# Optimization experiments

Measured on AMD Instinct MI355X. Metric: run time of the kernel, lower is better.

## Reference

```python
import jax, jax.numpy as jnp
import numpy as np

B, S, D_IN, D_H = 8, 4096, 256, 512
EPS = 1e-6


def setup_inputs() -> dict:
    key = jax.random.key(0)
    ks = jax.random.split(key, 5)
    scale = 1.0 / np.sqrt(D_IN)  # torch Linear default init scale (uniform bound)
    x = jax.random.normal(ks[0], (B, S, D_IN), dtype=jnp.float32)
    Wi = jax.random.normal(ks[1], (D_IN, D_H), dtype=jnp.float32) * scale
    Wf = jax.random.normal(ks[2], (D_IN, D_H), dtype=jnp.float32) * scale
    Wo = jax.random.normal(ks[3], (D_IN, D_H), dtype=jnp.float32) * scale
    Wz = jax.random.normal(ks[4], (D_IN, D_H), dtype=jnp.float32) * scale
    zb = jnp.zeros((D_H,), dtype=jnp.float32)
    return {"x": x, "Wi": Wi, "bi": zb, "Wf": Wf, "bf": zb,
            "Wo": Wo, "bo": zb, "Wz": Wz, "bz": zb}


def _xlstm_forward(x, Wi, bi, Wf, bf, Wo, bo, Wz, bz):
    # Batched projections over all timesteps at once: [B,S,D_H] each.
    i_t = jnp.exp(jnp.clip(jnp.einsum('bsd,dh->bsh', x, Wi) + bi, -20.0, 0.0))
    f_t = jnp.exp(jnp.clip(jnp.einsum('bsd,dh->bsh', x, Wf) + bf, -20.0, 0.0))
    o_t = jax.nn.sigmoid(jnp.einsum('bsd,dh->bsh', x, Wo) + bo)
    z_t = jnp.tanh(jnp.einsum('bsd,dh->bsh', x, Wz) + bz)

    def step(carry, gates):
        c, n = carry
        i, f, o, z = gates
        c = f * c + i * z
        n = f * n + i
        h = o * (c / (n + EPS))
        return (c, n), h

    c0 = jnp.zeros((x.shape[0], Wi.shape[1]), dtype=x.dtype)
    n0 = jnp.ones((x.shape[0], Wi.shape[1]), dtype=x.dtype)
    # time-major scan over the recurrence
    gates_tm = tuple(jnp.swapaxes(g, 0, 1) for g in (i_t, f_t, o_t, z_t))  # [S,B,H]
    _, h_tm = jax.lax.scan(step, (c0, n0), gates_tm)
    return jnp.swapaxes(h_tm, 0, 1)  # [B,S,H]


def reference(x, Wi, bi, Wf, bf, Wo, bo, Wz, bz):
    return _xlstm_forward(x, Wi, bi, Wf, bf, Wo, bo, Wz, bz)
```

## Files before the change

kernel.cpp:

```cpp
#include <hip/hip_runtime.h>
#include <hip/hip_bf16.h>
#include <cstdint>
#include <cstddef>

typedef __hip_bfloat16 bf16;
typedef __attribute__((ext_vector_type(8))) short short8;
typedef __attribute__((ext_vector_type(4))) short short4v;
typedef __attribute__((ext_vector_type(4))) float floatx4;

#define BB 8
#define SS 4096
#define DIN 256
#define DH 512
#define NCH 256
#define CHUNK 16

__device__ __forceinline__ float b2f(bf16 v) { return __bfloat162float(v); }
__device__ __forceinline__ float sh2f(short v) {
    unsigned int u = ((unsigned int)(unsigned short)v) << 16;
    float f; __builtin_memcpy(&f, &u, 4); return f;
}
__device__ __forceinline__ float frcp(float x) { return __builtin_amdgcn_rcpf(x); }
__device__ __forceinline__ short f2sh(float a) {
    bf16 bv = __float2bfloat16(a);
    short sv; __builtin_memcpy(&sv, &bv, 2); return sv;
}

__global__ __launch_bounds__(256) void convert_x(
    const float* __restrict__ X, bf16* __restrict__ Xb)
{
    const int idx = blockIdx.x * 256 + threadIdx.x;
    float4 v = ((const float4*)X)[idx];
    bf16 o[4] = {__float2bfloat16(v.x), __float2bfloat16(v.y),
                 __float2bfloat16(v.z), __float2bfloat16(v.w)};
    ((short4v*)Xb)[idx] = *(const short4v*)o;
}

__global__ __launch_bounds__(256) void transpose_w(
    const float* __restrict__ Wi, const float* __restrict__ Wf,
    const float* __restrict__ Wo, const float* __restrict__ Wz,
    bf16* __restrict__ Wt)
{
    int o = blockIdx.x * 256 + threadIdx.x;
    int r = o >> 8;
    int k = o & 255;
    int y = r >> 7;
    int c = r & 127;
    int g = c >> 5;
    int h = y * 32 + (c & 31);
    const float* W = (g == 0) ? Wi : (g == 1) ? Wf : (g == 2) ? Wo : Wz;
    Wt[o] = __float2bfloat16(W[(size_t)k * DH + h]);
}

__device__ __forceinline__ void load16_lds(const bf16* g, short* l)
{
    __builtin_amdgcn_global_load_lds(
        (const __attribute__((address_space(1))) unsigned int*)g,
        (__attribute__((address_space(3))) unsigned int*)l,
        16, 0, 0);
}

__global__ __launch_bounds__(256) void gemm_mfma(
    const bf16* __restrict__ Xb, const bf16* __restrict__ Wt,
    const float* __restrict__ bi, const float* __restrict__ bfv,
    const float* __restrict__ bo, const float* __restrict__ bz,
    bf16* __restrict__ Pi, bf16* __restrict__ Pf,
    bf16* __restrict__ Po, bf16* __restrict__ Pz,
    float* __restrict__ Aa, float* __restrict__ Bca, float* __restrict__ Bna,
    int nb)
{
    __shared__ __align__(16) short smem[128 * 132];

    const int tid  = threadIdx.x;
    const int y    = blockIdx.x;
    const int m0   = blockIdx.y * 128;
    const int n0   = y * 128;
    const int wave = tid >> 6, lane = tid & 63;
    const int wm   = (wave >> 1) * 64, wn = (wave & 1) * 64;
    const int l15  = lane & 15;
    const int q    = lane >> 4;

    floatx4 acc[4][4];
#pragma unroll
    for (int i = 0; i < 4; i++)
#pragma unroll
        for (int j = 0; j < 4; j++) acc[i][j] = (floatx4){0.f, 0.f, 0.f, 0.f};

    const int r_ld = tid >> 2;
    const int c_ld = tid & 3;
    const bf16* agp0 = Xb + (size_t)(m0 + r_ld) * DIN + c_ld * 8;
    const bf16* agp1 = Xb + (size_t)(m0 + 64 + r_ld) * DIN + c_ld * 8;
    const bf16* bgp0 = Wt + (size_t)(n0 + r_ld) * DIN + c_ld * 8;
    const bf16* bgp1 = Wt + (size_t)(n0 + 64 + r_ld) * DIN + c_ld * 8;

#define STAGE(K0, BUF)                                            \
    do {                                                          \
        short* A_ = smem + (BUF) * 8192;                          \
        short* B_ = A_ + 4096;                                    \
        load16_lds(agp0 + (K0), &A_[tid * 8]);                    \
        load16_lds(agp1 + (K0), &A_[2048 + tid * 8]);             \
        load16_lds(bgp0 + (K0), &B_[tid * 8]);                    \
        load16_lds(bgp1 + (K0), &B_[2048 + tid * 8]);             \
    } while (0)

    STAGE(0, 0);
    asm volatile("s_waitcnt vmcnt(0)" ::: "memory");
    __builtin_amdgcn_s_barrier();

#pragma unroll
    for (int k = 0; k < 8; k++) {
        const int cur = k & 1;
        if (k < 7) STAGE((k + 1) * 32, cur ^ 1);
        const short* A = smem + cur * 8192;
        const short* B = A + 4096;
        short8 af[4], bfr[4];
#pragma unroll
        for (int ti = 0; ti < 4; ti++)
            af[ti] = *(const short8*)&A[(wm + ti * 16 + l15) * 32 + q * 8];
#pragma unroll
        for (int tj = 0; tj < 4; tj++)
            bfr[tj] = *(const short8*)&B[(wn + tj * 16 + l15) * 32 + q * 8];
#pragma unroll
        for (int ti = 0; ti < 4; ti++)
#pragma unroll
            for (int tj = 0; tj < 4; tj++)
                acc[ti][tj] = __builtin_amdgcn_mfma_f32_16x16x32_bf16(
                    af[ti], bfr[tj], acc[ti][tj], 0, 0, 0);
        asm volatile("s_waitcnt vmcnt(0) lgkmcnt(0)" ::: "memory");
        __builtin_amdgcn_s_barrier();
    }
#undef STAGE

#pragma unroll
    for (int ti = 0; ti < 4; ti++) {
        const int mrow = wm + ti * 16 + q * 4;
#pragma unroll
        for (int tj = 0; tj < 4; tj++) {
            const int cb = wn + tj * 16;
            const int g  = cb >> 5;
            const int c  = cb + l15;
            const float* bp = (g == 0) ? bi : (g == 1) ? bfv
                            : (g == 2) ? bo : bz;
            const float bsv = bp[y * 32 + (c & 31)];
#pragma unroll
            for (int r = 0; r < 4; r++) {
                const float v = acc[ti][tj][r] + bsv;
                float a;
                if (g == 0 || g == 1) {
                    a = __expf(fminf(fmaxf(v, -20.f), 0.f));
                } else if (g == 2) {
                    a = frcp(1.f + __expf(-v));
                } else {
                    a = 1.f - 2.f * frcp(__expf(2.f * v) + 1.f);
                }
                smem[(mrow + r) * 132 + c] = f2sh(a);
            }
        }
    }
    __syncthreads();

    const int bidx = m0 / SS;

    {
        const int cp  = (tid & 31) * 4;
        const int g2  = cp >> 5;
        const int hb  = y * 32 + (cp & 31);
        bf16* pl = ((g2 == 0) ? Pi : (g2 == 1) ? Pf : (g2 == 2) ? Po : Pz) + hb;
        const int r0 = tid >> 5;
#pragma unroll
        for (int t = 0; t < 16; t++) {
            const int row = t * 8 + r0;
            short4v v = *(const short4v*)&smem[row * 132 + cp];
            *(short4v*)(pl + (size_t)(m0 + row) * DH) = v;
        }
    }

    {
        const int hh = tid & 31;
        const int ch = tid >> 5;
        float A = 1.f, Bc = 0.f, Bn = 0.f;
        const short* base = &smem[(ch * CHUNK) * 132];
#pragma unroll
        for (int s = 0; s < CHUNK; s++) {
            const short* rp = base + s * 132;
            const float iv = sh2f(rp[hh]);
            const float f  = sh2f(rp[32 + hh]);
            const float zv = sh2f(rp[96 + hh]);
            Bc = fmaf(f, Bc, iv * zv);
            Bn = fmaf(f, Bn, iv);
            A *= f;
        }
        const int ch_g = ((m0 % SS) >> 4) + ch;
        const int hgl  = y * 32 + hh;
        const size_t cidx = (size_t)(ch_g * nb + bidx) * DH + hgl;
        Aa[cidx] = A; Bca[cidx] = Bc; Bna[cidx] = Bn;
    }
}

__global__ __launch_bounds__(256) void scan_chunks(
    float* __restrict__ Aa, float* __restrict__ Bca,
    const float* __restrict__ Bna, int nb)
{
    const int t = blockIdx.x * 256 + threadIdx.x;
    float c = 0.f, n = 1.f;
    for (int ch = 0; ch < NCH; ch++) {
        const size_t cidx = (size_t)ch * (nb * DH) + t;
        const float A  = Aa[cidx];
        const float Bc = Bca[cidx];
        const float Bn = Bna[cidx];
        Aa[cidx] = c; Bca[cidx] = n;
        c = fmaf(A, c, Bc);
        n = fmaf(A, n, Bn);
    }
}

__global__ __launch_bounds__(256) void scan_emit(
    const bf16* __restrict__ Pi, const bf16* __restrict__ Pf,
    const bf16* __restrict__ Po, const bf16* __restrict__ Pz,
    const float* __restrict__ Cs, const float* __restrict__ Ns,
    float* __restrict__ out, int nb)
{
    const int tid = threadIdx.x;
    const int ch  = blockIdx.x * 4 + (tid >> 6);
    const int b   = blockIdx.y;
    const int hg  = (tid & 63) * 8;
    const size_t base = ((size_t)(b * SS + ch * CHUNK)) * DH + hg;
    const size_t cidx = (size_t)(ch * nb + b) * DH + hg;

    float c[8], n[8];
#pragma unroll
    for (int j = 0; j < 2; j++) {
        *(floatx4*)&c[j * 4] = *(const floatx4*)(Cs + cidx + j * 4);
        *(floatx4*)&n[j * 4] = *(const floatx4*)(Ns + cidx + j * 4);
    }

#pragma unroll 4
    for (int s = 0; s < CHUNK; s++) {
        const size_t o = base + (size_t)s * DH;
        short8 i8 = *(const short8*)(Pi + o);
        short8 f8 = *(const short8*)(Pf + o);
        short8 o8 = *(const short8*)(Po + o);
        short8 z8 = *(const short8*)(Pz + o);
        float h[8];
#pragma unroll
        for (int j = 0; j < 8; j++) {
            const float f  = sh2f(f8[j]);
            const float iv = sh2f(i8[j]);
            const float ov = sh2f(o8[j]);
            const float zv = sh2f(z8[j]);
            c[j] = fmaf(f, c[j], iv * zv);
            n[j] = fmaf(f, n[j], iv);
            h[j] = ov * c[j] * frcp(n[j] + 1e-6f);
        }
        *(floatx4*)(out + o)     = *(floatx4*)&h[0];
        *(floatx4*)(out + o + 4) = *(floatx4*)&h[4];
    }
}

extern "C" void kernel_launch(void* const* d_in, const int* in_sizes, int n_in,
                              void* d_out, int out_size, void* d_ws, size_t ws_size,
                              hipStream_t stream)
{
    const float* x   = (const float*)d_in[0];
    const float* Wi  = (const float*)d_in[1];
    const float* bi  = (const float*)d_in[2];
    const float* Wf  = (const float*)d_in[3];
    const float* bfv = (const float*)d_in[4];
    const float* Wo  = (const float*)d_in[5];
    const float* bo  = (const float*)d_in[6];
    const float* Wz  = (const float*)d_in[7];
    const float* bz  = (const float*)d_in[8];
    float* out = (float*)d_out;

    int nb = BB;
    while (nb > 1) {
        size_t need = (1u << 20)
                    + (size_t)nb * SS * DIN * 2
                    + 4 * (size_t)nb * SS * DH * 2
                    + 3 * (size_t)NCH * nb * DH * 4;
        if (need <= ws_size) break;
        nb >>= 1;
    }

    const size_t plane = (size_t)nb * SS * DH;
    bf16* Wt = (bf16*)d_ws;
    bf16* Xb = (bf16*)((char*)d_ws + (1u << 20));
    bf16* Pi = Xb + (size_t)nb * SS * DIN;
    bf16* Pf = Pi + plane;
    bf16* Po = Pf + plane;
    bf16* Pz = Po + plane;
    float* Aa  = (float*)(Pz + plane);
    float* Bca = Aa  + (size_t)NCH * nb * DH;
    float* Bna = Bca + (size_t)NCH * nb * DH;

    transpose_w<<<2048, 256, 0, stream>>>(Wi, Wf, Wo, Wz, Wt);

    for (int b0 = 0; b0 < BB; b0 += nb) {
        const float* Xsrc = x   + (size_t)b0 * SS * DIN;
        float*       Ob   = out + (size_t)b0 * SS * DH;
        convert_x<<<nb * 1024, 256, 0, stream>>>(Xsrc, Xb);
        gemm_mfma<<<dim3(16, nb * SS / 128), 256, 0, stream>>>(
            Xb, Wt, bi, bfv, bo, bz, Pi, Pf, Po, Pz, Aa, Bca, Bna, nb);
        scan_chunks<<<2 * nb, 256, 0, stream>>>(Aa, Bca, Bna, nb);
        scan_emit<<<dim3(NCH / 4, nb), 256, 0, stream>>>(
            Pi, Pf, Po, Pz, Aa, Bca, Ob, nb);
    }
}
```

Measured before the change: 253.9 us.

## Triple-buffer GEMM loads, swizzle block order, parallelize chunk scan, widen emit grid

The GEMM moves from double to triple buffering with partial vmcnt waits, so global-to-LDS loads for two stages ahead overlap the MFMA work. It also remaps block indices across 8 groups, likely an XCD-aware swizzle. The chunk-state scan splits its 256 chunks into 4 segments per hidden lane and combines them through shared memory, giving more blocks and a shorter serial chain. scan_emit now handles 4 channels per thread with twice as many blocks, trading narrower vector loads for more parallelism.

```diff
diff --git a/kernel.cpp b/kernel.cpp
--- a/kernel.cpp
+++ b/kernel.cpp
@@ -69,12 +69,15 @@
     float* __restrict__ Aa, float* __restrict__ Bca, float* __restrict__ Bna,
     int nb)
 {
-    __shared__ __align__(16) short smem[128 * 132];
+    __shared__ __align__(16) short smem[3 * 8192];
+
+    const int cpx = gridDim.x >> 3;
+    const int logical = ((int)blockIdx.x & 7) * cpx + ((int)blockIdx.x >> 3);
+    const int y  = logical & 15;
+    const int m0 = (logical >> 4) * 128;
+    const int n0 = y * 128;
 
     const int tid  = threadIdx.x;
-    const int y    = blockIdx.x;
-    const int m0   = blockIdx.y * 128;
-    const int n0   = y * 128;
     const int wave = tid >> 6, lane = tid & 63;
     const int wm   = (wave >> 1) * 64, wn = (wave & 1) * 64;
     const int l15  = lane & 15;
@@ -104,14 +107,18 @@
     } while (0)
 
     STAGE(0, 0);
-    asm volatile("s_waitcnt vmcnt(0)" ::: "memory");
-    __builtin_amdgcn_s_barrier();
+    STAGE(32, 1);
 
 #pragma unroll
     for (int k = 0; k < 8; k++) {
-        const int cur = k & 1;
-        if (k < 7) STAGE((k + 1) * 32, cur ^ 1);
-        const short* A = smem + cur * 8192;
+        if (k < 6) STAGE((k + 2) * 32, (k + 2) % 3);
+        if (k < 6)       asm volatile("s_waitcnt vmcnt(8)" ::: "memory");
+        else if (k == 6) asm volatile("s_waitcnt vmcnt(4)" ::: "memory");
+        else             asm volatile("s_waitcnt vmcnt(0)" ::: "memory");
+        __builtin_amdgcn_s_barrier();
+        __builtin_amdgcn_sched_barrier(0);
+
+        const short* A = smem + (k % 3) * 8192;
         const short* B = A + 4096;
         short8 af[4], bfr[4];
 #pragma unroll
@@ -126,7 +133,8 @@
             for (int tj = 0; tj < 4; tj++)
                 acc[ti][tj] = __builtin_amdgcn_mfma_f32_16x16x32_bf16(
                     af[ti], bfr[tj], acc[ti][tj], 0, 0, 0);
-        asm volatile("s_waitcnt vmcnt(0) lgkmcnt(0)" ::: "memory");
+        asm volatile("s_waitcnt lgkmcnt(0)" ::: "memory");
+        __builtin_amdgcn_sched_barrier(0);
         __builtin_amdgcn_s_barrier();
     }
 #undef STAGE
@@ -201,16 +209,46 @@
     float* __restrict__ Aa, float* __restrict__ Bca,
     const float* __restrict__ Bna, int nb)
 {
-    const int t = blockIdx.x * 256 + threadIdx.x;
+    __shared__ float sA[4][64], sBc[4][64], sBn[4][64];
+    const int tid = threadIdx.x;
+    const int t   = blockIdx.x * 64 + (tid & 63);
+    const int s   = tid >> 6;
+    const int stride = nb * DH;
+    const int SEG = NCH / 4;
+
+    float A = 1.f, Bc = 0.f, Bn = 0.f;
+    for (int k = 0; k < SEG; k++) {
+        const size_t cidx = (size_t)(s * SEG + k) * stride + t;
+        const float a  = Aa[cidx];
+        const float bc = Bca[cidx];
+        const float bn = Bna[cidx];
+        Bc = fmaf(a, Bc, bc);
+        Bn = fmaf(a, Bn, bn);
+        A *= a;
+    }
+    sA[s][tid & 63] = A; sBc[s][tid & 63] = Bc; sBn[s][tid & 63] = Bn;
+    __syncthreads();
+
     float c = 0.f, n = 1.f;
-    for (int ch = 0; ch < NCH; ch++) {
-        const size_t cidx = (size_t)ch * (nb * DH) + t;
-        const float A  = Aa[cidx];
-        const float Bc = Bca[cidx];
-        const float Bn = Bna[cidx];
+#pragma unroll
+    for (int s2 = 0; s2 < 3; s2++) {
+        if (s2 < s) {
+            const float a  = sA[s2][tid & 63];
+            const float nc = fmaf(a, c, sBc[s2][tid & 63]);
+            n = fmaf(a, n, sBn[s2][tid & 63]);
+            c = nc;
+        }
+    }
+
+    for (int k = 0; k < SEG; k++) {
+        const size_t cidx = (size_t)(s * SEG + k) * stride + t;
+        const float a  = Aa[cidx];
+        const float bc = Bca[cidx];
+        const float bn = Bna[cidx];
         Aa[cidx] = c; Bca[cidx] = n;
-        c = fmaf(A, c, Bc);
-        n = fmaf(A, n, Bn);
+        const float nc = fmaf(a, c, bc);
+        n = fmaf(a, n, bn);
+        c = nc;
     }
 }
 
@@ -221,39 +259,35 @@
     float* __restrict__ out, int nb)
 {
     const int tid = threadIdx.x;
-    const int ch  = blockIdx.x * 4 + (tid >> 6);
+    const int ch  = blockIdx.x * 2 + (tid >> 7);
     const int b   = blockIdx.y;
-    const int hg  = (tid & 63) * 8;
+    const int hg  = (tid & 127) * 4;
     const size_t base = ((size_t)(b * SS + ch * CHUNK)) * DH + hg;
     const size_t cidx = (size_t)(ch * nb + b) * DH + hg;
 
-    float c[8], n[8];
-#pragma unroll
-    for (int j = 0; j < 2; j++) {
-        *(floatx4*)&c[j * 4] = *(const floatx4*)(Cs + cidx + j * 4);
-        *(floatx4*)&n[j * 4] = *(const floatx4*)(Ns + cidx + j * 4);
-    }
+    float c[4], n[4];
+    *(floatx4*)c = *(const floatx4*)(Cs + cidx);
+    *(floatx4*)n = *(const floatx4*)(Ns + cidx);
 
 #pragma unroll 4
     for (int s = 0; s < CHUNK; s++) {
         const size_t o = base + (size_t)s * DH;
-        short8 i8 = *(const short8*)(Pi + o);
-        short8 f8 = *(const short8*)(Pf + o);
-        short8 o8 = *(const short8*)(Po + o);
-        short8 z8 = *(const short8*)(Pz + o);
-        float h[8];
-#pragma unroll
-        for (int j = 0; j < 8; j++) {
-            const float f  = sh2f(f8[j]);
-            const float iv = sh2f(i8[j]);
-            const float ov = sh2f(o8[j]);
-            const float zv = sh2f(z8[j]);
+        short4v i4 = *(const short4v*)(Pi + o);
+        short4v f4 = *(const short4v*)(Pf + o);
+        short4v o4 = *(const short4v*)(Po + o);
+        short4v z4 = *(const short4v*)(Pz + o);
+        float h[4];
+#pragma unroll
+        for (int j = 0; j < 4; j++) {
+            const float f  = sh2f(f4[j]);
+            const float iv = sh2f(i4[j]);
+            const float ov = sh2f(o4[j]);
+            const float zv = sh2f(z4[j]);
             c[j] = fmaf(f, c[j], iv * zv);
             n[j] = fmaf(f, n[j], iv);
             h[j] = ov * c[j] * frcp(n[j] + 1e-6f);
         }
-        *(floatx4*)(out + o)     = *(floatx4*)&h[0];
-        *(floatx4*)(out + o + 4) = *(floatx4*)&h[4];
+        *(floatx4*)(out + o) = *(floatx4*)h;
     }
 }
 
@@ -299,10 +333,10 @@
         const float* Xsrc = x   + (size_t)b0 * SS * DIN;
         float*       Ob   = out + (size_t)b0 * SS * DH;
         convert_x<<<nb * 1024, 256, 0, stream>>>(Xsrc, Xb);
-        gemm_mfma<<<dim3(16, nb * SS / 128), 256, 0, stream>>>(
+        gemm_mfma<<<nb * 512, 256, 0, stream>>>(
             Xb, Wt, bi, bfv, bo, bz, Pi, Pf, Po, Pz, Aa, Bca, Bna, nb);
-        scan_chunks<<<2 * nb, 256, 0, stream>>>(Aa, Bca, Bna, nb);
-        scan_emit<<<dim3(NCH / 4, nb), 256, 0, stream>>>(
+        scan_chunks<<<nb * 8, 256, 0, stream>>>(Aa, Bca, Bna, nb);
+        scan_emit<<<dim3(NCH / 2, nb), 256, 0, stream>>>(
             Pi, Pf, Po, Pz, Aa, Bca, Ob, nb);
     }
 }
```

New measurement: 233.2 us. 8.1% less time.
